# Optimization experiments

Hardware: AMD Instinct MI355X
Metric: run time of the kernel (lower is better)

## Reference

```python
import jax, jax.numpy as jnp
import numpy as np

N_NODES = 100000
N_EDGES = 1600000
IN_CH = 61
OUT_CH = 64
BN_EPS = 1e-5


def setup_inputs() -> dict:
    key = jax.random.key(0)
    ks = jax.random.split(key, 8)
    x = jax.random.normal(ks[0], (N_NODES, IN_CH), dtype=jnp.float32)
    pos = jax.random.normal(ks[1], (N_NODES, 3), dtype=jnp.float32)
    edge_index = jax.random.randint(ks[2], (2, N_EDGES), 0, N_NODES, dtype=jnp.int64)
    d_in = 3 + IN_CH  # 64
    W1 = jax.random.normal(ks[3], (d_in, OUT_CH), dtype=jnp.float32) / np.sqrt(d_in)
    b1 = jnp.zeros((OUT_CH,), dtype=jnp.float32)
    g1 = jnp.ones((OUT_CH,), dtype=jnp.float32)
    be1 = jnp.zeros((OUT_CH,), dtype=jnp.float32)
    Wg = jax.random.normal(ks[4], (OUT_CH, 1), dtype=jnp.float32) / np.sqrt(OUT_CH)
    bg = jnp.zeros((1,), dtype=jnp.float32)
    gg = jnp.ones((1,), dtype=jnp.float32)
    bgb = jnp.zeros((1,), dtype=jnp.float32)
    return {"x": x, "pos": pos, "edge_index": edge_index,
            "W1": W1, "b1": b1, "g1": g1, "be1": be1,
            "Wg": Wg, "bg": bg, "gg": gg, "bgb": bgb}


def _bn_act(h, gamma, beta):
    # PyG MLP layer: BatchNorm1d (training-mode batch stats) -> SiLU
    mu = h.mean(axis=0)
    var = h.var(axis=0)
    h = (h - mu) * jax.lax.rsqrt(var + BN_EPS) * gamma + beta
    return jax.nn.silu(h)


def reference(x, pos, edge_index, W1, b1, g1, be1, Wg, bg, gg, bgb):
    src = edge_index[0]  # source node j (messages flow j -> i)
    dst = edge_index[1]  # target node i
    n = x.shape[0]
    # PointNetConv message: local_nn(cat([x_j, pos_j - pos_i]))
    feat = jnp.concatenate([x[src], pos[src] - pos[dst]], axis=-1)  # [E, 3+in]
    h = _bn_act(feat @ W1 + b1, g1, be1)  # [E, out]
    # AttentionalAggregation gate: MLP([out, 1]) per edge
    gate = _bn_act(h @ Wg + bg, gg, bgb)  # [E, 1]
    # segment softmax over destination nodes
    m = jax.ops.segment_max(gate, dst, num_segments=n)  # [N, 1]
    e = jnp.exp(gate - m[dst])
    s = jax.ops.segment_sum(e, dst, num_segments=n)
    alpha = e / (s[dst] + 1e-16)
    # weighted scatter-sum aggregate
    out = jax.ops.segment_sum(alpha * h, dst, num_segments=n)  # [N, out]
    return out
```

## Files before the change

kernel.cpp:

```cpp
#include <hip/hip_runtime.h>
#include <hip/hip_bf16.h>
#include <hip/hip_fp16.h>
#include <math.h>

constexpr int N_NODES = 100000;
constexpr int N_EDGES = 1600000;
constexpr int IN_CH   = 61;
constexpr float BN_EPS = 1e-5f;
constexpr int NPART   = 32;

constexpr int S_PH = 192;
constexpr int S_PG = 192 + NPART * 128;
constexpr int S_TOT = S_PG + NPART * 2;

typedef float f32x4 __attribute__((ext_vector_type(4)));
typedef short s16x8 __attribute__((ext_vector_type(8)));

__device__ __forceinline__ float fast_exp(float x) { return __expf(x); }
__device__ __forceinline__ float silu(float x) {
    return x * __builtin_amdgcn_rcpf(1.0f + __expf(-x));
}

__device__ __forceinline__ float bf2f(unsigned v) { return __uint_as_float(v << 16); }
__device__ __forceinline__ unsigned f2bf(float f) {
    unsigned u = __float_as_uint(f);
    return (u + 0x7FFFu + ((u >> 16) & 1u)) >> 16;
}

__device__ __forceinline__ bool edge_gemm(
    int e, const float* __restrict__ x, const float* __restrict__ pos,
    const int* __restrict__ ei, const float* __restrict__ W1,
    const float* __restrict__ b1, float* acc, int* jd_out)
{
    int js = ei[e];
    int jd = ei[N_EDGES + e];
    *jd_out = jd;
    bool valid = ((unsigned)js < (unsigned)N_NODES) && ((unsigned)jd < (unsigned)N_NODES);
    if (!valid) {
        #pragma unroll
        for (int c = 0; c < 64; ++c) acc[c] = 0.0f;
        return false;
    }
    #pragma unroll
    for (int c = 0; c < 64; ++c) acc[c] = b1[c];
    const float* xr = x + (size_t)js * IN_CH;
    #pragma unroll 4
    for (int k = 0; k < IN_CH; ++k) {
        float fk = xr[k];
        #pragma unroll
        for (int c = 0; c < 64; ++c) acc[c] += fk * W1[k * 64 + c];
    }
    #pragma unroll
    for (int j = 0; j < 3; ++j) {
        float fk = pos[js * 3 + j] - pos[jd * 3 + j];
        #pragma unroll
        for (int c = 0; c < 64; ++c) acc[c] += fk * W1[(IN_CH + j) * 64 + c];
    }
    return true;
}

__global__ __launch_bounds__(256) void k_init(float* stats, int* deg) {
    int i = blockIdx.x * 256 + threadIdx.x;
    if (i < S_TOT) stats[i] = 0.0f;
    if (i < N_NODES) deg[i] = 0;
}

__global__ __launch_bounds__(256) void k_prep(const float* __restrict__ W1,
                                              short* __restrict__ wf)
{
    int i = blockIdx.x * 256 + threadIdx.x;
    int j    = i & 7;
    int lane = (i >> 3) & 63;
    int kc   = (i >> 9) & 1;
    int ct   = i >> 10;
    int c = ct * 16 + (lane & 15);
    int k = kc * 32 + (lane >> 4) * 8 + j;
    float v = W1[k * 64 + c];
    unsigned hi = f2bf(v);
    unsigned lo = f2bf(v - bf2f(hi));
    wf[i] = (short)hi;
    wf[4096 + i] = (short)lo;
}

__global__ __launch_bounds__(256) void k_edge_mfma(
    const float* __restrict__ x, const float* __restrict__ pos,
    const int* __restrict__ ei, const short* __restrict__ wf,
    const float* __restrict__ b1, float* __restrict__ stats,
    int* __restrict__ deg, void* __restrict__ h, size_t h_cap)
{
    __shared__ __align__(16) short fsh[64][72];
    __shared__ __align__(16) short fsl[64][72];
    __shared__ float lsum[128];

    const int tid  = threadIdx.x;
    const int w    = tid >> 6, lane = tid & 63;
    const int e0   = blockIdx.x * 64;

    if (tid < 128) lsum[tid] = 0.0f;

    int js_l = 0, jd_l = 0;
    if (lane < 16) {
        int e = e0 + w * 16 + lane;
        js_l = ei[e];
        jd_l = ei[N_EDGES + e];
        if ((unsigned)js_l >= (unsigned)N_NODES) js_l = 0;
        if ((unsigned)jd_l >= (unsigned)N_NODES) jd_l = 0;
        atomicAdd(&deg[jd_l], 1);
    }

    #pragma unroll 4
    for (int j = 0; j < 16; ++j) {
        int js = __shfl(js_l, j);
        int jd = __shfl(jd_l, j);
        int r  = w * 16 + j;
        float v;
        if (lane < IN_CH) v = x[(size_t)js * IN_CH + lane];
        else              v = pos[js * 3 + (lane - IN_CH)] - pos[jd * 3 + (lane - IN_CH)];
        unsigned hi = f2bf(v);
        unsigned lo = f2bf(v - bf2f(hi));
        fsh[r][lane] = (short)hi;
        fsl[r][lane] = (short)lo;
    }
    __syncthreads();

    const int r = lane & 15, g = lane >> 4;
    const int arow = w * 16 + r;
    s16x8 ah0 = *(const s16x8*)&fsh[arow][g * 8];
    s16x8 ah1 = *(const s16x8*)&fsh[arow][32 + g * 8];
    s16x8 al0 = *(const s16x8*)&fsl[arow][g * 8];
    s16x8 al1 = *(const s16x8*)&fsl[arow][32 + g * 8];

    const bool do_h = ((size_t)(e0 + 64) * 128 <= h_cap);
    unsigned short* hp = (unsigned short*)h;

    #pragma unroll
    for (int ct = 0; ct < 4; ++ct) {
        int c = ct * 16 + r;
        s16x8 bh0 = *(const s16x8*)&wf[((ct * 2 + 0) * 64 + lane) * 8];
        s16x8 bh1 = *(const s16x8*)&wf[((ct * 2 + 1) * 64 + lane) * 8];
        s16x8 bl0 = *(const s16x8*)&wf[4096 + ((ct * 2 + 0) * 64 + lane) * 8];
        s16x8 bl1 = *(const s16x8*)&wf[4096 + ((ct * 2 + 1) * 64 + lane) * 8];
        f32x4 acc = {0.0f, 0.0f, 0.0f, 0.0f};
        acc = __builtin_amdgcn_mfma_f32_16x16x32_bf16(al0, bh0, acc, 0, 0, 0);
        acc = __builtin_amdgcn_mfma_f32_16x16x32_bf16(al1, bh1, acc, 0, 0, 0);
        acc = __builtin_amdgcn_mfma_f32_16x16x32_bf16(ah0, bl0, acc, 0, 0, 0);
        acc = __builtin_amdgcn_mfma_f32_16x16x32_bf16(ah1, bl1, acc, 0, 0, 0);
        acc = __builtin_amdgcn_mfma_f32_16x16x32_bf16(ah0, bh0, acc, 0, 0, 0);
        acc = __builtin_amdgcn_mfma_f32_16x16x32_bf16(ah1, bh1, acc, 0, 0, 0);
        float bias = b1[c];
        float s = 0.0f, q = 0.0f;
        #pragma unroll
        for (int i = 0; i < 4; ++i) {
            unsigned hb = f2bf(acc[i] + bias);
            float v = bf2f(hb);
            s += v; q += v * v;
            if (do_h) {
                int row = w * 16 + g * 4 + i;
                hp[(size_t)(e0 + row) * 64 + c] = (unsigned short)hb;
            }
        }
        s += __shfl_xor(s, 16); s += __shfl_xor(s, 32);
        q += __shfl_xor(q, 16); q += __shfl_xor(q, 32);
        if (g == 0) {
            atomicAdd(&lsum[c], s);
            atomicAdd(&lsum[64 + c], q);
        }
    }
    __syncthreads();
    if (tid < 128)
        atomicAdd(&stats[S_PH + (blockIdx.x & (NPART - 1)) * 128 + tid], lsum[tid]);
}

template<int MODE>
__global__ __launch_bounds__(128) void k_edge(
    const float* __restrict__ x, const float* __restrict__ pos,
    const int* __restrict__ ei, const float* __restrict__ W1,
    const float* __restrict__ b1, float* __restrict__ stats,
    int* __restrict__ deg, void* __restrict__ h, size_t h_cap)
{
    constexpr int EPB = 128;
    __shared__ float fs[EPB][65];
    __shared__ float ls[128];

    const int tid  = threadIdx.x;
    const int wave = tid >> 6, lane = tid & 63;
    const int eb   = blockIdx.x * EPB;
    const int r0   = wave * 64;

    const int eg = eb + r0 + lane;
    int js_l = ei[eg];
    int jd_l = ei[N_EDGES + eg];
    bool valid = ((unsigned)js_l < (unsigned)N_NODES) &&
                 ((unsigned)jd_l < (unsigned)N_NODES);
    if (valid) atomicAdd(&deg[jd_l], 1);

    if constexpr (MODE == 2) {
        if (tid < 128) ls[tid] = 0.0f;
    }

    for (int j = 0; j < 64; ++j) {
        int js = __shfl(js_l, j);
        int jd = __shfl(jd_l, j);
        int ok = __shfl((int)valid, j);
        int r = r0 + j;
        if (lane < IN_CH) {
            fs[r][lane] = ok ? x[(size_t)js * IN_CH + lane] : 0.0f;
        } else {
            int d = lane - IN_CH;
            fs[r][lane] = ok ? (pos[js * 3 + d] - pos[jd * 3 + d]) : 0.0f;
        }
    }
    __syncthreads();

    #pragma unroll 1
    for (int half = 0; half < 2; ++half) {
        const int base = half * 32;
        float acc[32];
        #pragma unroll
        for (int c = 0; c < 32; ++c) acc[c] = valid ? b1[base + c] : 0.0f;
        if (valid) {
            #pragma unroll 4
            for (int k = 0; k < 64; ++k) {
                float fk = fs[tid][k];
                #pragma unroll
                for (int c = 0; c < 32; ++c)
                    acc[c] += fk * W1[k * 64 + base + c];
            }
        }
        if constexpr (MODE == 0) {
            if ((size_t)(eb + tid + 1) * 256 <= h_cap) {
                float4* hq = (float4*)((char*)h + (size_t)(eb + tid) * 256
                                       + (size_t)base * 4);
                #pragma unroll
                for (int i = 0; i < 8; ++i)
                    hq[i] = make_float4(acc[4*i], acc[4*i+1], acc[4*i+2], acc[4*i+3]);
            }
        } else {
            #pragma unroll
            for (int c = 0; c < 32; ++c) {
                atomicAdd(&ls[base + c], acc[c]);
                atomicAdd(&ls[64 + base + c], acc[c] * acc[c]);
            }
        }
    }

    if constexpr (MODE == 2) {
        __syncthreads();
        if (tid < 128)
            atomicAdd(&stats[S_PH + (blockIdx.x & (NPART-1)) * 128 + tid], ls[tid]);
    }
}

template<int MODE>
__global__ __launch_bounds__(256) void k_stats(const void* __restrict__ h,
                                               float* __restrict__ stats)
{
    constexpr int VEC = (MODE == 0) ? 4 : 8;
    const size_t nvec = (size_t)N_EDGES * 64 / VEC;
    size_t stride = (size_t)gridDim.x * 256;
    size_t g0 = (size_t)blockIdx.x * 256 + threadIdx.x;
    int c0 = (int)((g0 * VEC) & 63);
    float sum[VEC], sq[VEC];
    #pragma unroll
    for (int j = 0; j < VEC; ++j) { sum[j] = 0.0f; sq[j] = 0.0f; }

    for (size_t v = g0; v < nvec; v += stride) {
        float vals[VEC];
        if constexpr (MODE == 0) {
            float4 t = ((const float4*)h)[v];
            vals[0] = t.x; vals[1] = t.y; vals[2] = t.z; vals[3] = t.w;
        } else {
            uint4 t = ((const uint4*)h)[v];
            vals[0] = bf2f(t.x & 0xFFFF); vals[1] = bf2f(t.x >> 16);
            vals[2] = bf2f(t.y & 0xFFFF); vals[3] = bf2f(t.y >> 16);
            vals[4] = bf2f(t.z & 0xFFFF); vals[5] = bf2f(t.z >> 16);
            vals[6] = bf2f(t.w & 0xFFFF); vals[7] = bf2f(t.w >> 16);
        }
        #pragma unroll
        for (int j = 0; j < VEC; ++j) { sum[j] += vals[j]; sq[j] += vals[j] * vals[j]; }
    }
    __shared__ float ls[128];
    if (threadIdx.x < 128) ls[threadIdx.x] = 0.0f;
    __syncthreads();
    #pragma unroll
    for (int j = 0; j < VEC; ++j) {
        atomicAdd(&ls[c0 + j], sum[j]);
        atomicAdd(&ls[64 + c0 + j], sq[j]);
    }
    __syncthreads();
    if (threadIdx.x < 128)
        atomicAdd(&stats[S_PH + (blockIdx.x & (NPART-1)) * 128 + threadIdx.x],
                  ls[threadIdx.x]);
}

__global__ void k_bnfin(float* stats) {
    int c = threadIdx.x;
    if (c < 64) {
        float s = 0.0f, q = 0.0f;
        #pragma unroll
        for (int p = 0; p < NPART; ++p) {
            s += stats[S_PH + p * 128 + c];
            q += stats[S_PH + p * 128 + 64 + c];
        }
        float m = s / (float)N_EDGES;
        float v = q / (float)N_EDGES - m * m;
        stats[c] = m;
        stats[64 + c] = rsqrtf(v + BN_EPS);
    }
}

template<int MODE>
__global__ __launch_bounds__(256) void k_gate(
    void* __restrict__ h, const float* __restrict__ x,
    const float* __restrict__ pos, const int* __restrict__ ei,
    const float* __restrict__ W1, const float* __restrict__ b1,
    float* __restrict__ stats, const float* __restrict__ g1,
    const float* __restrict__ be1, const float* __restrict__ Wg,
    const float* __restrict__ bg, float* __restrict__ gate_lin, size_t h_cap)
{
    int e = blockIdx.x * 256 + threadIdx.x;
    float gl = bg[0];

    if constexpr (MODE == 2) {
        float hv[64];
        int jd;
        edge_gemm(e, x, pos, ei, W1, b1, hv, &jd);
        #pragma unroll
        for (int c = 0; c < 64; ++c) {
            float t = (hv[c] - stats[c]) * stats[64 + c] * g1[c] + be1[c];
            gl += silu(t) * Wg[c];
        }
    } else if constexpr (MODE == 0) {
        if ((size_t)(e + 1) * 256 <= h_cap) {
            float4* hq = (float4*)((char*)h + (size_t)e * 256);
            #pragma unroll
            for (int i = 0; i < 16; ++i) {
                float4 t = hq[i];
                float vv[4] = {t.x, t.y, t.z, t.w};
                float sv[4];
                #pragma unroll
                for (int j = 0; j < 4; ++j) {
                    int c = 4 * i + j;
                    float tt = (vv[j] - stats[c]) * stats[64 + c] * g1[c] + be1[c];
                    sv[j] = silu(tt);
                    gl += sv[j] * Wg[c];
                }
                hq[i] = make_float4(sv[0], sv[1], sv[2], sv[3]);
            }
        }
    } else {
        if ((size_t)(e + 1) * 128 <= h_cap) {
            uint4* hq = (uint4*)((char*)h + (size_t)e * 128);
            #pragma unroll
            for (int j = 0; j < 8; ++j) {
                uint4 t = hq[j];
                float vv[8];
                vv[0] = bf2f(t.x & 0xFFFF); vv[1] = bf2f(t.x >> 16);
                vv[2] = bf2f(t.y & 0xFFFF); vv[3] = bf2f(t.y >> 16);
                vv[4] = bf2f(t.z & 0xFFFF); vv[5] = bf2f(t.z >> 16);
                vv[6] = bf2f(t.w & 0xFFFF); vv[7] = bf2f(t.w >> 16);
                unsigned pw[4];
                #pragma unroll
                for (int q = 0; q < 4; ++q) {
                    int c0 = 8 * j + 2 * q;
                    float t0 = (vv[2*q]   - stats[c0])   * stats[64 + c0]   * g1[c0]   + be1[c0];
                    float t1 = (vv[2*q+1] - stats[c0+1]) * stats[64 + c0+1] * g1[c0+1] + be1[c0+1];
                    float s0 = silu(t0), s1 = silu(t1);
                    gl += s0 * Wg[c0] + s1 * Wg[c0 + 1];
                    unsigned u0 = __half_as_ushort(__float2half(s0));
                    unsigned u1 = __half_as_ushort(__float2half(s1));
                    pw[q] = u0 | (u1 << 16);
                }
                hq[j] = make_uint4(pw[0], pw[1], pw[2], pw[3]);
            }
        }
    }
    gate_lin[e] = gl;

    float s1 = gl, s2 = gl * gl;
    #pragma unroll
    for (int off = 32; off >= 1; off >>= 1) {
        s1 += __shfl_xor(s1, off);
        s2 += __shfl_xor(s2, off);
    }
    __shared__ float red[8];
    int w = threadIdx.x >> 6, lane = threadIdx.x & 63;
    if (lane == 0) { red[w] = s1; red[4 + w] = s2; }
    __syncthreads();
    if (threadIdx.x == 0) {
        int slot = S_PG + (blockIdx.x & (NPART-1)) * 2;
        atomicAdd(&stats[slot], red[0] + red[1] + red[2] + red[3]);
        atomicAdd(&stats[slot + 1], red[4] + red[5] + red[6] + red[7]);
    }
}

__global__ void k_gfin(float* stats) {
    if (threadIdx.x == 0) {
        float s = 0.0f, q = 0.0f;
        for (int p = 0; p < NPART; ++p) {
            s += stats[S_PG + 2 * p];
            q += stats[S_PG + 2 * p + 1];
        }
        float m = s / (float)N_EDGES;
        float v = q / (float)N_EDGES - m * m;
        stats[128] = m;
        stats[129] = rsqrtf(v + BN_EPS);
    }
}

__global__ __launch_bounds__(256) void k_w(float* __restrict__ gate_lin,
                                           const float* __restrict__ stats,
                                           const float* __restrict__ gg,
                                           const float* __restrict__ bgb)
{
    int e = blockIdx.x * 256 + threadIdx.x;
    float gl = gate_lin[e];
    float tg = (gl - stats[128]) * stats[129] * gg[0] + bgb[0];
    gate_lin[e] = fast_exp(silu(tg));
}

__global__ __launch_bounds__(1024) void k_scan(const int* __restrict__ deg,
                                               int* __restrict__ offs,
                                               int* __restrict__ cursor)
{
    __shared__ int ps[1024];
    int t = threadIdx.x;
    const int CH = (N_NODES + 1023) / 1024;
    int lo = t * CH, hi = lo + CH;
    if (hi > N_NODES) hi = N_NODES;
    if (lo > N_NODES) lo = N_NODES;
    int s = 0;
    for (int i = lo; i < hi; ++i) s += deg[i];
    ps[t] = s;
    __syncthreads();
    for (int off = 1; off < 1024; off <<= 1) {
        int v = (t >= off) ? ps[t - off] : 0;
        __syncthreads();
        ps[t] += v;
        __syncthreads();
    }
    int run = (t == 0) ? 0 : ps[t - 1];
    for (int i = lo; i < hi; ++i) {
        offs[i] = run;
        cursor[i] = run;
        run += deg[i];
    }
    if (t == 1023) offs[N_NODES] = ps[1023];
}

__global__ __launch_bounds__(256) void k_fill(const int* __restrict__ ei,
                                              int* __restrict__ cursor,
                                              int* __restrict__ elist)
{
    int e = blockIdx.x * 256 + threadIdx.x;
    int js = ei[e];
    int d = ei[N_EDGES + e];
    if ((unsigned)js >= (unsigned)N_NODES || (unsigned)d >= (unsigned)N_NODES) return;
    int p = atomicAdd(&cursor[d], 1);
    if ((unsigned)p < (unsigned)N_EDGES) elist[p] = e;
}

template<int MODE>
__device__ __forceinline__ void aggr_body(
    const void* __restrict__ h, size_t h_cap, const float* __restrict__ wgt,
    const int* __restrict__ offs, const int* __restrict__ elist,
    const int* __restrict__ ei, const float* __restrict__ x,
    const float* __restrict__ pos, const float* __restrict__ b1,
    const float* W1s, const float* __restrict__ stats,
    const float* __restrict__ g1, const float* __restrict__ be1,
    float* __restrict__ out)
{
    int wid = (blockIdx.x * 256 + threadIdx.x) >> 6;
    int lane = threadIdx.x & 63;
    if (wid >= N_NODES) return;

    int lo = offs[wid], hi = offs[wid + 1];
    float accv = 0.0f, wsum = 0.0f;

    if constexpr (MODE == 2) {
        float mu = stats[lane], rs = stats[64 + lane];
        float ga = g1[lane], bb = be1[lane];
        float b1v = b1[lane];
        float pim = (lane >= IN_CH) ? pos[wid * 3 + (lane - IN_CH)] : 0.0f;
        for (int i = lo; i < hi; ++i) {
            int e = elist[i];
            float w = wgt[e];
            int js = ei[e];
            if ((unsigned)js >= (unsigned)N_NODES) continue;
            float fl = (lane < IN_CH) ? x[(size_t)js * IN_CH + lane]
                                      : pos[js * 3 + (lane - IN_CH)] - pim;
            float a = b1v;
            #pragma unroll
            for (int k = 0; k < 64; ++k) a += __shfl(fl, k) * W1s[k * 64 + lane];
            float tn = (a - mu) * rs * ga + bb;
            accv += w * silu(tn);
            wsum += w;
        }
    } else {
        auto load_h = [&](int e) -> float {
            if constexpr (MODE == 0) {
                if ((size_t)(e + 1) * 256 > h_cap) return 0.0f;
                return ((const float*)h)[(size_t)e * 64 + lane];
            } else {
                if ((size_t)(e + 1) * 128 > h_cap) return 0.0f;
                return __half2float(__ushort_as_half(
                    ((const unsigned short*)h)[(size_t)e * 64 + lane]));
            }
        };
        if (lo < hi) {
            int e = elist[lo];
            float w = wgt[e];
            float hval = load_h(e);
            for (int i = lo; i < hi; ++i) {
                int en = 0; float wn = 0.0f, hn = 0.0f;
                if (i + 1 < hi) {
                    en = elist[i + 1];
                    wn = wgt[en];
                    hn = load_h(en);
                }
                accv += w * hval;
                wsum += w;
                e = en; w = wn; hval = hn;
            }
        }
    }
    out[(size_t)wid * 64 + lane] = accv / (wsum + 1e-16f);
}

template<int MODE>
__global__ __launch_bounds__(256) void k_aggr(
    const void* __restrict__ h, size_t h_cap, const float* __restrict__ wgt,
    const int* __restrict__ offs, const int* __restrict__ elist,
    const int* __restrict__ ei, const float* __restrict__ x,
    const float* __restrict__ pos, const float* __restrict__ b1,
    const float* __restrict__ W1, const float* __restrict__ stats,
    const float* __restrict__ g1, const float* __restrict__ be1,
    float* __restrict__ out)
{
    if constexpr (MODE == 2) {
        __shared__ float W1s[4096];
        for (int i = threadIdx.x; i < 4096; i += 256) W1s[i] = W1[i];
        __syncthreads();
        aggr_body<2>(h, h_cap, wgt, offs, elist, ei, x, pos, b1, W1s,
                     stats, g1, be1, out);
    } else {
        aggr_body<MODE>(h, h_cap, wgt, offs, elist, ei, x, pos, b1, nullptr,
                        stats, g1, be1, out);
    }
}

extern "C" void kernel_launch(void* const* d_in, const int* in_sizes, int n_in,
                              void* d_out, int out_size, void* d_ws, size_t ws_size,
                              hipStream_t stream)
{
    const float* x   = (const float*)d_in[0];
    const float* pos = (const float*)d_in[1];
    const int*   ei  = (const int*)d_in[2];
    const float* W1  = (const float*)d_in[3];
    const float* b1  = (const float*)d_in[4];
    const float* g1  = (const float*)d_in[5];
    const float* be1 = (const float*)d_in[6];
    const float* Wg  = (const float*)d_in[7];
    const float* bg  = (const float*)d_in[8];
    const float* gg  = (const float*)d_in[9];
    const float* bgb = (const float*)d_in[10];
    float* out = (float*)d_out;

    char* base = (char*)d_ws;
    size_t off = 0;
    auto alloc = [&](size_t bytes) {
        size_t o = off;
        off = (off + bytes + 255) & ~(size_t)255;
        return o;
    };
    float* stats    = (float*)(base + alloc(S_TOT * 4));
    int*   deg      = (int*)(base + alloc((size_t)N_NODES * 4));
    int*   offs     = (int*)(base + alloc((size_t)(N_NODES + 1) * 4));
    int*   cursor   = (int*)(base + alloc((size_t)N_NODES * 4));
    int*   elist    = (int*)(base + alloc((size_t)N_EDGES * 4));
    float* gate_lin = (float*)(base + alloc((size_t)N_EDGES * 4));
    short* wfrag    = (short*)(base + alloc(8192 * 2));
    if (ws_size < off) return;
    void*  h     = (void*)(base + off);
    size_t h_cap = ws_size - off;

    const int mode = (h_cap >= (size_t)N_EDGES * 256) ? 0
                   : (h_cap >= (size_t)N_EDGES * 128) ? 1 : 2;

    const int EB  = N_EDGES / 256;
    const int EB2 = N_EDGES / 128;
    const int EBM = N_EDGES / 64;
    const int NB  = (N_NODES + 255) / 256;
    const int AB  = (N_NODES + 3) / 4;

    hipLaunchKernelGGL(k_init, dim3(NB), dim3(256), 0, stream, stats, deg);

    if (mode == 0) {
        hipLaunchKernelGGL(k_edge<0>, dim3(EB2), dim3(128), 0, stream,
                           x, pos, ei, W1, b1, stats, deg, h, h_cap);
        hipLaunchKernelGGL(k_stats<0>, dim3(1024), dim3(256), 0, stream, h, stats);
        hipLaunchKernelGGL(k_bnfin, dim3(1), dim3(64), 0, stream, stats);
        hipLaunchKernelGGL(k_gate<0>, dim3(EB), dim3(256), 0, stream,
                           h, x, pos, ei, W1, b1, stats, g1, be1, Wg, bg, gate_lin, h_cap);
    } else if (mode == 1) {
        hipLaunchKernelGGL(k_prep, dim3(16), dim3(256), 0, stream, W1, wfrag);
        hipLaunchKernelGGL(k_edge_mfma, dim3(EBM), dim3(256), 0, stream,
                           x, pos, ei, wfrag, b1, stats, deg, h, h_cap);
        hipLaunchKernelGGL(k_bnfin, dim3(1), dim3(64), 0, stream, stats);
        hipLaunchKernelGGL(k_gate<1>, dim3(EB), dim3(256), 0, stream,
                           h, x, pos, ei, W1, b1, stats, g1, be1, Wg, bg, gate_lin, h_cap);
    } else {
        hipLaunchKernelGGL(k_edge<2>, dim3(EB2), dim3(128), 0, stream,
                           x, pos, ei, W1, b1, stats, deg, h, h_cap);
        hipLaunchKernelGGL(k_bnfin, dim3(1), dim3(64), 0, stream, stats);
        hipLaunchKernelGGL(k_gate<2>, dim3(EB), dim3(256), 0, stream,
                           h, x, pos, ei, W1, b1, stats, g1, be1, Wg, bg, gate_lin, h_cap);
    }

    hipLaunchKernelGGL(k_gfin, dim3(1), dim3(64), 0, stream, stats);
    hipLaunchKernelGGL(k_w,    dim3(EB), dim3(256), 0, stream, gate_lin, stats, gg, bgb);
    hipLaunchKernelGGL(k_scan, dim3(1), dim3(1024), 0, stream, deg, offs, cursor);
    hipLaunchKernelGGL(k_fill, dim3(EB), dim3(256), 0, stream, ei, cursor, elist);

    if (mode == 0) {
        hipLaunchKernelGGL(k_aggr<0>, dim3(AB), dim3(256), 0, stream,
                           h, h_cap, gate_lin, offs, elist, ei, x, pos, b1, W1,
                           stats, g1, be1, out);
    } else if (mode == 1) {
        hipLaunchKernelGGL(k_aggr<1>, dim3(AB), dim3(256), 0, stream,
                           h, h_cap, gate_lin, offs, elist, ei, x, pos, b1, W1,
                           stats, g1, be1, out);
    } else {
        hipLaunchKernelGGL(k_aggr<2>, dim3(AB), dim3(256), 0, stream,
                           h, h_cap, gate_lin, offs, elist, ei, x, pos, b1, W1,
                           stats, g1, be1, out);
    }
}
```

Before: 985.2 us.

## Stop writing activated h back; recompute BN+SiLU in aggregation and fuse gate exp into fill

The gate kernel now only reads the pre-activation h and no longer writes the normalized/SiLU'd activations back. Aggregation instead recomputes the BN and SiLU per lane from the raw h, which now stays in bf16 rather than being rewritten as fp16. The standalone k_w pass that turned gate logits into exp weights is folded into k_fill, removing one kernel launch and one pass over gate_lin. This trades a full E x 64 write of h for extra per-edge transcendental work in aggregation.

```diff
diff --git a/kernel.cpp b/kernel.cpp
--- a/kernel.cpp
+++ b/kernel.cpp
@@ -311,7 +311,7 @@
 
 template<int MODE>
 __global__ __launch_bounds__(256) void k_gate(
-    void* __restrict__ h, const float* __restrict__ x,
+    const void* __restrict__ h, const float* __restrict__ x,
     const float* __restrict__ pos, const int* __restrict__ ei,
     const float* __restrict__ W1, const float* __restrict__ b1,
     float* __restrict__ stats, const float* __restrict__ g1,
@@ -332,25 +332,22 @@
         }
     } else if constexpr (MODE == 0) {
         if ((size_t)(e + 1) * 256 <= h_cap) {
-            float4* hq = (float4*)((char*)h + (size_t)e * 256);
+            const float4* hq = (const float4*)((const char*)h + (size_t)e * 256);
             #pragma unroll
             for (int i = 0; i < 16; ++i) {
                 float4 t = hq[i];
                 float vv[4] = {t.x, t.y, t.z, t.w};
-                float sv[4];
                 #pragma unroll
                 for (int j = 0; j < 4; ++j) {
                     int c = 4 * i + j;
                     float tt = (vv[j] - stats[c]) * stats[64 + c] * g1[c] + be1[c];
-                    sv[j] = silu(tt);
-                    gl += sv[j] * Wg[c];
+                    gl += silu(tt) * Wg[c];
                 }
-                hq[i] = make_float4(sv[0], sv[1], sv[2], sv[3]);
             }
         }
     } else {
         if ((size_t)(e + 1) * 128 <= h_cap) {
-            uint4* hq = (uint4*)((char*)h + (size_t)e * 128);
+            const uint4* hq = (const uint4*)((const char*)h + (size_t)e * 128);
             #pragma unroll
             for (int j = 0; j < 8; ++j) {
                 uint4 t = hq[j];
@@ -359,19 +356,12 @@
                 vv[2] = bf2f(t.y & 0xFFFF); vv[3] = bf2f(t.y >> 16);
                 vv[4] = bf2f(t.z & 0xFFFF); vv[5] = bf2f(t.z >> 16);
                 vv[6] = bf2f(t.w & 0xFFFF); vv[7] = bf2f(t.w >> 16);
-                unsigned pw[4];
                 #pragma unroll
-                for (int q = 0; q < 4; ++q) {
-                    int c0 = 8 * j + 2 * q;
-                    float t0 = (vv[2*q]   - stats[c0])   * stats[64 + c0]   * g1[c0]   + be1[c0];
-                    float t1 = (vv[2*q+1] - stats[c0+1]) * stats[64 + c0+1] * g1[c0+1] + be1[c0+1];
-                    float s0 = silu(t0), s1 = silu(t1);
-                    gl += s0 * Wg[c0] + s1 * Wg[c0 + 1];
-                    unsigned u0 = __half_as_ushort(__float2half(s0));
-                    unsigned u1 = __half_as_ushort(__float2half(s1));
-                    pw[q] = u0 | (u1 << 16);
+                for (int q = 0; q < 8; ++q) {
+                    int c = 8 * j + q;
+                    float tt = (vv[q] - stats[c]) * stats[64 + c] * g1[c] + be1[c];
+                    gl += silu(tt) * Wg[c];
                 }
-                hq[j] = make_uint4(pw[0], pw[1], pw[2], pw[3]);
             }
         }
     }
@@ -406,17 +396,6 @@
         stats[128] = m;
         stats[129] = rsqrtf(v + BN_EPS);
     }
-}
-
-__global__ __launch_bounds__(256) void k_w(float* __restrict__ gate_lin,
-                                           const float* __restrict__ stats,
-                                           const float* __restrict__ gg,
-                                           const float* __restrict__ bgb)
-{
-    int e = blockIdx.x * 256 + threadIdx.x;
-    float gl = gate_lin[e];
-    float tg = (gl - stats[128]) * stats[129] * gg[0] + bgb[0];
-    gate_lin[e] = fast_exp(silu(tg));
 }
 
 __global__ __launch_bounds__(1024) void k_scan(const int* __restrict__ deg,
@@ -450,9 +429,17 @@
 
 __global__ __launch_bounds__(256) void k_fill(const int* __restrict__ ei,
                                               int* __restrict__ cursor,
-                                              int* __restrict__ elist)
+                                              int* __restrict__ elist,
+                                              float* __restrict__ gate_lin,
+                                              const float* __restrict__ stats,
+                                              const float* __restrict__ gg,
+                                              const float* __restrict__ bgb)
 {
     int e = blockIdx.x * 256 + threadIdx.x;
+    float gl = gate_lin[e];
+    float tg = (gl - stats[128]) * stats[129] * gg[0] + bgb[0];
+    gate_lin[e] = fast_exp(silu(tg));
+
     int js = ei[e];
     int d = ei[N_EDGES + e];
     if ((unsigned)js >= (unsigned)N_NODES || (unsigned)d >= (unsigned)N_NODES) return;
@@ -474,12 +461,13 @@
     int lane = threadIdx.x & 63;
     if (wid >= N_NODES) return;
 
+    float mu = stats[lane], rs = stats[64 + lane];
+    float ga = g1[lane], bb = be1[lane];
+
     int lo = offs[wid], hi = offs[wid + 1];
     float accv = 0.0f, wsum = 0.0f;
 
     if constexpr (MODE == 2) {
-        float mu = stats[lane], rs = stats[64 + lane];
-        float ga = g1[lane], bb = be1[lane];
         float b1v = b1[lane];
         float pim = (lane >= IN_CH) ? pos[wid * 3 + (lane - IN_CH)] : 0.0f;
         for (int i = lo; i < hi; ++i) {
@@ -503,8 +491,7 @@
                 return ((const float*)h)[(size_t)e * 64 + lane];
             } else {
                 if ((size_t)(e + 1) * 128 > h_cap) return 0.0f;
-                return __half2float(__ushort_as_half(
-                    ((const unsigned short*)h)[(size_t)e * 64 + lane]));
+                return bf2f(((const unsigned short*)h)[(size_t)e * 64 + lane]);
             }
         };
         if (lo < hi) {
@@ -518,7 +505,8 @@
                     wn = wgt[en];
                     hn = load_h(en);
                 }
-                accv += w * hval;
+                float tn = (hval - mu) * rs * ga + bb;
+                accv += w * silu(tn);
                 wsum += w;
                 e = en; w = wn; hval = hn;
             }
@@ -618,9 +606,9 @@
     }
 
     hipLaunchKernelGGL(k_gfin, dim3(1), dim3(64), 0, stream, stats);
-    hipLaunchKernelGGL(k_w,    dim3(EB), dim3(256), 0, stream, gate_lin, stats, gg, bgb);
     hipLaunchKernelGGL(k_scan, dim3(1), dim3(1024), 0, stream, deg, offs, cursor);
-    hipLaunchKernelGGL(k_fill, dim3(EB), dim3(256), 0, stream, ei, cursor, elist);
+    hipLaunchKernelGGL(k_fill, dim3(EB), dim3(256), 0, stream,
+                       ei, cursor, elist, gate_lin, stats, gg, bgb);
 
     if (mode == 0) {
         hipLaunchKernelGGL(k_aggr<0>, dim3(AB), dim3(256), 0, stream,
```

Result: no change. 967.2 us (-1.8%).
